# Kernel optimization log

Measured on AMD Instinct MI355X. Metric: run time of the kernel, lower is better.

Reference implementation:

```python
import jax, jax.numpy as jnp
import numpy as np
from jax import lax

L = 128       # layers_num (sequential recurrence length)
D = 262144    # input_dim


def setup_inputs() -> dict:
    key = jax.random.key(0)
    ks = jax.random.split(key, 7)
    x = jax.random.normal(ks[0], (L, D), dtype=jnp.float32)
    weight_x = jax.random.normal(ks[1], (L, D), dtype=jnp.float32) * 0.1 + 1.0
    weight_g = jax.random.normal(ks[2], (L, D), dtype=jnp.float32) * 0.1 + 1.0
    weight_u = jax.random.normal(ks[3], (L, D), dtype=jnp.float32) * 0.1 + 1.0
    mask = jax.random.uniform(ks[4], (L, D), dtype=jnp.float32)
    fc_w = jax.random.normal(ks[5], (1, D), dtype=jnp.float32) * (1.0 / np.sqrt(D))
    fc_b = jax.random.normal(ks[6], (1,), dtype=jnp.float32) * 0.01
    return {"x": x, "weight_x": weight_x, "weight_g": weight_g,
            "weight_u": weight_u, "mask": mask, "fc_w": fc_w, "fc_b": fc_b}


def reference(x, weight_x, weight_g, weight_u, mask, fc_w, fc_b):
    sg = lax.stop_gradient
    # t = 0 initialization (mirrors the .detach() calls in the torch code)
    xbar0 = sg(x[0])                              # x_bar[0]
    h0 = jnp.tanh(sg(x[0]) * weight_x[0])         # h[0]
    xbar1 = sg(h0) * weight_g[0] + x[0]           # x_bar[1]

    def step(carry, inp):
        h_prev, xbar_t = carry                    # h[t-1], x_bar[t], each [D]
        xt, mt, wxt, wut, wgt = inp
        x_trans = xt * mt + xbar_t * (1.0 - mt)
        u = jnp.tanh(x_trans * wxt)
        f = jax.nn.sigmoid(sg(h_prev) + u * wut) * mt
        h_t = f * h_prev + (1.0 - f) * u
        h_t = h0 + jax.nn.relu(h_t - h0)
        xbar_next = sg(h_t) * wgt + sg(x_trans)   # x_bar[t+1]
        return (h_t, xbar_next), xbar_t

    xs = (x[1:], mask[1:], weight_x[1:], weight_u[1:], weight_g[1:])
    _, xbar_seq = lax.scan(step, (h0, xbar1), xs)  # x_bar[1..L-1], [L-1, D]
    x_bar = jnp.concatenate([xbar0[None], xbar_seq], axis=0)  # [L, D]
    pred = jax.nn.sigmoid(x_bar @ fc_w.T + fc_b)   # [L, 1]
    return pred
```

## Files before the change

### kernel.cpp

```cpp
#include <hip/hip_runtime.h>


#define L     128
#define DCOLS 262144
#define TPB   256
#define NWAVE (TPB / 64)
#define NBLK  (DCOLS / (2 * TPB))

__device__ __forceinline__ float wred(float v) {
#pragma unroll
    for (int o = 32; o > 0; o >>= 1) v += __shfl_xor(v, o, 64);
    return v;
}

__device__ __forceinline__ float rcpf(float x) { return __builtin_amdgcn_rcpf(x); }

__device__ __forceinline__ float ftanh(float a) {
    a = fminf(fmaxf(a, -15.f), 15.f);
    float e = __expf(-2.f * a);
    return (1.f - e) * rcpf(1.f + e);
}

__device__ __forceinline__ float fsig(float z) {
    return rcpf(1.f + __expf(-z));
}

__global__ __launch_bounds__(TPB) void rnn_main(
    const float* __restrict__ x,  const float* __restrict__ wx,
    const float* __restrict__ wg, const float* __restrict__ wu,
    const float* __restrict__ m,  const float* __restrict__ fcw,
    float* __restrict__ part)
{
    __shared__ float lacc[NWAVE][L];
    const int tid  = threadIdx.x;
    const int lane = tid & 63;
    const int wid  = tid >> 6;
    const int col2 = blockIdx.x * TPB + tid;
    const int stride2 = DCOLS / 2;

    const float2* px  = (const float2*)x  + col2;
    const float2* pm  = (const float2*)m  + col2;
    const float2* pwx = (const float2*)wx + col2;
    const float2* pwu = (const float2*)wu + col2;
    const float2* pwg = (const float2*)wg + col2;

    const float2 fw = ((const float2*)fcw)[col2];

    float2 x0  = px[0];
    float2 wx0 = pwx[0];
    float2 wg0 = pwg[0];

    float2 h0, h, xb;
    h0.x = ftanh(x0.x * wx0.x);  h0.y = ftanh(x0.y * wx0.y);
    xb.x = h0.x * wg0.x + x0.x;  xb.y = h0.y * wg0.y + x0.y;
    h = h0;

    {
        float s = wred(x0.x * fw.x + x0.y * fw.y);
        if (lane == 0) lacc[wid][0] = s;
    }

    float2 xn  = px[stride2];
    float2 mn  = pm[stride2];
    float2 wxn = pwx[stride2];
    float2 wun = pwu[stride2];
    float2 wgn = pwg[stride2];

    for (int t = 1; t < L; ++t) {
        float2 xc = xn, mc = mn, wxc = wxn, wuc = wun, wgc = wgn;
        if (t < L - 1) {
            const int o = (t + 1) * stride2;
            xn = px[o]; mn = pm[o]; wxn = pwx[o]; wun = pwu[o]; wgn = pwg[o];
        }

        float s = wred(xb.x * fw.x + xb.y * fw.y);
        if (lane == 0) lacc[wid][t] = s;

        {
            float xt = xc.x * mc.x + xb.x * (1.f - mc.x);
            float u  = ftanh(xt * wxc.x);
            float f  = fsig(h.x + u * wuc.x) * mc.x;
            float hn = f * h.x + (1.f - f) * u;
            h.x  = fmaxf(hn, h0.x);
            xb.x = h.x * wgc.x + xt;
        }
        {
            float xt = xc.y * mc.y + xb.y * (1.f - mc.y);
            float u  = ftanh(xt * wxc.y);
            float f  = fsig(h.y + u * wuc.y) * mc.y;
            float hn = f * h.y + (1.f - f) * u;
            h.y  = fmaxf(hn, h0.y);
            xb.y = h.y * wgc.y + xt;
        }
    }

    __syncthreads();
    if (tid < L) {
        float s = 0.f;
#pragma unroll
        for (int w = 0; w < NWAVE; ++w) s += lacc[w][tid];
        part[blockIdx.x * L + tid] = s;
    }
}

__global__ __launch_bounds__(64) void rnn_finish(
    const float* __restrict__ part, const float* __restrict__ fcb,
    float* __restrict__ out)
{
    const int t    = blockIdx.x;
    const int lane = threadIdx.x;
    float s = 0.f;
    for (int b = lane; b < NBLK; b += 64) s += part[b * L + t];
    s = wred(s);
    if (lane == 0) out[t] = fsig(s + fcb[0]);
}

extern "C" void kernel_launch(void* const* d_in, const int* in_sizes, int n_in,
                              void* d_out, int out_size, void* d_ws, size_t ws_size,
                              hipStream_t stream) {
    const float* x   = (const float*)d_in[0];
    const float* wx  = (const float*)d_in[1];
    const float* wg  = (const float*)d_in[2];
    const float* wu  = (const float*)d_in[3];
    const float* m   = (const float*)d_in[4];
    const float* fcw = (const float*)d_in[5];
    const float* fcb = (const float*)d_in[6];
    float* out  = (float*)d_out;
    float* part = (float*)d_ws;

    rnn_main<<<NBLK, TPB, 0, stream>>>(x, wx, wg, wu, m, fcw, part);
    rnn_finish<<<L, 64, 0, stream>>>(part, fcb, out);
}
```

Baseline: 114.6 us.

## Use one column per thread with two-step-ahead software prefetch

Each thread now handles a single column instead of a float2 pair, which doubles the number of blocks to 1024 of 256 threads. Loads are prefetched two timesteps ahead using alternating A/B register sets, with the loop unrolled by two. The goal is more waves and more loads in flight to hide memory latency in this bandwidth-bound recurrence. The cost is a shuffle reduction per column-pair instead of per pair-sum, twice as many partial sums in the finish kernel, and narrower scalar loads.

```diff
diff --git a/kernel.cpp b/kernel.cpp
--- a/kernel.cpp
+++ b/kernel.cpp
@@ -5,7 +5,7 @@
 #define DCOLS 262144
 #define TPB   256
 #define NWAVE (TPB / 64)
-#define NBLK  (DCOLS / (2 * TPB))
+#define NBLK  (DCOLS / TPB)
 
 __device__ __forceinline__ float wred(float v) {
 #pragma unroll
@@ -35,64 +35,67 @@
     const int tid  = threadIdx.x;
     const int lane = tid & 63;
     const int wid  = tid >> 6;
-    const int col2 = blockIdx.x * TPB + tid;
-    const int stride2 = DCOLS / 2;
+    const int col  = blockIdx.x * TPB + tid;
 
-    const float2* px  = (const float2*)x  + col2;
-    const float2* pm  = (const float2*)m  + col2;
-    const float2* pwx = (const float2*)wx + col2;
-    const float2* pwu = (const float2*)wu + col2;
-    const float2* pwg = (const float2*)wg + col2;
+    const float* px  = x  + col;
+    const float* pm  = m  + col;
+    const float* pwx = wx + col;
+    const float* pwu = wu + col;
+    const float* pwg = wg + col;
 
-    const float2 fw = ((const float2*)fcw)[col2];
+    const float fw = fcw[col];
 
-    float2 x0  = px[0];
-    float2 wx0 = pwx[0];
-    float2 wg0 = pwg[0];
+    float x0  = px[0];
+    float wx0 = pwx[0];
+    float wg0 = pwg[0];
 
-    float2 h0, h, xb;
-    h0.x = ftanh(x0.x * wx0.x);  h0.y = ftanh(x0.y * wx0.y);
-    xb.x = h0.x * wg0.x + x0.x;  xb.y = h0.y * wg0.y + x0.y;
-    h = h0;
+    float h0 = ftanh(x0 * wx0);
+    float h  = h0;
+    float xb = h0 * wg0 + x0;
 
     {
-        float s = wred(x0.x * fw.x + x0.y * fw.y);
+        float s = wred(x0 * fw);
         if (lane == 0) lacc[wid][0] = s;
     }
 
-    float2 xn  = px[stride2];
-    float2 mn  = pm[stride2];
-    float2 wxn = pwx[stride2];
-    float2 wun = pwu[stride2];
-    float2 wgn = pwg[stride2];
+    float Ax = px[DCOLS],  Am = pm[DCOLS],  Awx = pwx[DCOLS],
+          Awu = pwu[DCOLS], Awg = pwg[DCOLS];
+    float Bx = px[2*DCOLS], Bm = pm[2*DCOLS], Bwx = pwx[2*DCOLS],
+          Bwu = pwu[2*DCOLS], Bwg = pwg[2*DCOLS];
 
-    for (int t = 1; t < L; ++t) {
-        float2 xc = xn, mc = mn, wxc = wxn, wuc = wun, wgc = wgn;
-        if (t < L - 1) {
-            const int o = (t + 1) * stride2;
-            xn = px[o]; mn = pm[o]; wxn = pwx[o]; wun = pwu[o]; wgn = pwg[o];
-        }
+#define STEP(T, XR, MR, WXR, WUR, WGR)                                   \
+    {                                                                    \
+        float s = wred(xb * fw);                      \
+        if (lane == 0) lacc[wid][(T)] = s;                               \
+        float xt = (XR) * (MR) + xb * (1.f - (MR));                      \
+        float u  = ftanh(xt * (WXR));                                    \
+        float f  = fsig(h + u * (WUR)) * (MR);                           \
+        float hn = f * h + (1.f - f) * u;                                \
+        h  = fmaxf(hn, h0);                         \
+        xb = h * (WGR) + xt;                                             \
+    }
 
-        float s = wred(xb.x * fw.x + xb.y * fw.y);
-        if (lane == 0) lacc[wid][t] = s;
-
+    int t = 1;
+    for (; t + 1 < L; t += 2) {
         {
-            float xt = xc.x * mc.x + xb.x * (1.f - mc.x);
-            float u  = ftanh(xt * wxc.x);
-            float f  = fsig(h.x + u * wuc.x) * mc.x;
-            float hn = f * h.x + (1.f - f) * u;
-            h.x  = fmaxf(hn, h0.x);
-            xb.x = h.x * wgc.x + xt;
+            float xc = Ax, mc = Am, wxc = Awx, wuc = Awu, wgc = Awg;
+            if (t + 2 < L) {
+                const long o = (long)(t + 2) * DCOLS;
+                Ax = px[o]; Am = pm[o]; Awx = pwx[o]; Awu = pwu[o]; Awg = pwg[o];
+            }
+            STEP(t, xc, mc, wxc, wuc, wgc);
         }
         {
-            float xt = xc.y * mc.y + xb.y * (1.f - mc.y);
-            float u  = ftanh(xt * wxc.y);
-            float f  = fsig(h.y + u * wuc.y) * mc.y;
-            float hn = f * h.y + (1.f - f) * u;
-            h.y  = fmaxf(hn, h0.y);
-            xb.y = h.y * wgc.y + xt;
+            float xc = Bx, mc = Bm, wxc = Bwx, wuc = Bwu, wgc = Bwg;
+            if (t + 3 < L) {
+                const long o = (long)(t + 3) * DCOLS;
+                Bx = px[o]; Bm = pm[o]; Bwx = pwx[o]; Bwu = pwu[o]; Bwg = pwg[o];
+            }
+            STEP(t + 1, xc, mc, wxc, wuc, wgc);
         }
     }
+    STEP(t, Ax, Am, Awx, Awu, Awg);
+#undef STEP
 
     __syncthreads();
     if (tid < L) {
```

Result: slower. 121.7 us (+6.2%).

## Fuse final reduction into main kernel via last-block atomic counter

Applied to the files above, without the earlier changes.

Removes the separate finish kernel: each block writes its partial sums transposed (time-major), then increments a global atomic counter, and the last block to finish reduces all partials and writes the sigmoid outputs. This is meant to save a kernel launch and its gap, and the transposed layout makes the final reads coalesced. In exchange it adds a memset launch for the counter, thread fences in every block, and a serial tail where a single block reduces 128x512 values.

```diff
diff --git a/kernel.cpp b/kernel.cpp
--- a/kernel.cpp
+++ b/kernel.cpp
@@ -6,6 +6,7 @@
 #define TPB   256
 #define NWAVE (TPB / 64)
 #define NBLK  (DCOLS / (2 * TPB))
+#define PART_BYTES (NBLK * L * 4)
 
 __device__ __forceinline__ float wred(float v) {
 #pragma unroll
@@ -29,9 +30,12 @@
     const float* __restrict__ x,  const float* __restrict__ wx,
     const float* __restrict__ wg, const float* __restrict__ wu,
     const float* __restrict__ m,  const float* __restrict__ fcw,
-    float* __restrict__ part)
+    const float* __restrict__ fcb,
+    float* __restrict__ part, unsigned int* __restrict__ counter,
+    float* __restrict__ out)
 {
     __shared__ float lacc[NWAVE][L];
+    __shared__ int   sIsLast;
     const int tid  = threadIdx.x;
     const int lane = tid & 63;
     const int wid  = tid >> 6;
@@ -99,20 +103,27 @@
         float s = 0.f;
 #pragma unroll
         for (int w = 0; w < NWAVE; ++w) s += lacc[w][tid];
-        part[blockIdx.x * L + tid] = s;
+        part[tid * NBLK + blockIdx.x] = s;
     }
-}
 
-__global__ __launch_bounds__(64) void rnn_finish(
-    const float* __restrict__ part, const float* __restrict__ fcb,
-    float* __restrict__ out)
-{
-    const int t    = blockIdx.x;
-    const int lane = threadIdx.x;
-    float s = 0.f;
-    for (int b = lane; b < NBLK; b += 64) s += part[b * L + t];
-    s = wred(s);
-    if (lane == 0) out[t] = fsig(s + fcb[0]);
+    __threadfence();
+    __syncthreads();
+    if (tid == 0) {
+        unsigned int old = atomicAdd(counter, 1u);
+        sIsLast = (old == NBLK - 1);
+    }
+    __syncthreads();
+    if (!sIsLast) return;
+
+    __threadfence();
+    const float bias = fcb[0];
+    for (int t = wid * (L / NWAVE); t < (wid + 1) * (L / NWAVE); ++t) {
+        float s = 0.f;
+#pragma unroll
+        for (int i = 0; i < NBLK / 64; ++i) s += part[t * NBLK + i * 64 + lane];
+        s = wred(s);
+        if (lane == 0) out[t] = fsig(s + bias);
+    }
 }
 
 extern "C" void kernel_launch(void* const* d_in, const int* in_sizes, int n_in,
@@ -127,7 +138,9 @@
     const float* fcb = (const float*)d_in[6];
     float* out  = (float*)d_out;
     float* part = (float*)d_ws;
+    unsigned int* counter = (unsigned int*)((char*)d_ws + PART_BYTES);
 
-    rnn_main<<<NBLK, TPB, 0, stream>>>(x, wx, wg, wu, m, fcw, part);
-    rnn_finish<<<L, 64, 0, stream>>>(part, fcb, out);
+    hipMemsetAsync(counter, 0, sizeof(unsigned int), stream);
+    rnn_main<<<NBLK, TPB, 0, stream>>>(x, wx, wg, wu, m, fcw, fcb,
+                                       part, counter, out);
 }
```

Measured after the change: 199.1 us. +73.8%, slower.
